# Performance work log

Measured on AMD Instinct MI355X. Metric: run time of the kernel, lower is better.

The kernel has to match this reference:

```python
import jax, jax.numpy as jnp
import numpy as np

B, S, D = 1, 2048, 2048
H, KVH, HD = 16, 8, 128
ROPE_THETA = 1e6
P_POW, C_SHIFT = 8, 7.0
MASK_VAL = -7.0  # = -c so masked bpmax base ~ scores only (finite under ^8)


def rotate_half(x):
    x1, x2 = jnp.split(x, 2, axis=-1)
    return jnp.concatenate([-x2, x1], axis=-1)


def setup_inputs() -> dict:
    key = jax.random.key(0)
    ks = jax.random.split(key, 10)
    hidden_states = jax.random.normal(ks[0], (B, S, D), dtype=jnp.float32)
    # RoPE tables (Qwen3-style, theta=1e6)
    inv_freq = 1.0 / (ROPE_THETA ** (jnp.arange(0, HD, 2, dtype=jnp.float32) / HD))
    freqs = jnp.arange(S, dtype=jnp.float32)[:, None] * inv_freq[None, :]
    emb = jnp.concatenate([freqs, freqs], axis=-1)  # [S, HD]
    cos = jnp.broadcast_to(jnp.cos(emb)[None], (B, S, HD)).astype(jnp.float32)
    sin = jnp.broadcast_to(jnp.sin(emb)[None], (B, S, HD)).astype(jnp.float32)
    sc = D ** -0.5
    q_proj_w = jax.random.normal(ks[1], (D, H * HD), dtype=jnp.float32) * sc
    k_proj_w = jax.random.normal(ks[2], (D, KVH * HD), dtype=jnp.float32) * sc
    v_proj_w = jax.random.normal(ks[3], (D, KVH * HD), dtype=jnp.float32) * sc
    o_proj_w = jax.random.normal(ks[4], (H * HD, D), dtype=jnp.float32) * (H * HD) ** -0.5
    q_norm_w = jnp.ones((HD,), dtype=jnp.float32)
    k_norm_w = jnp.ones((HD,), dtype=jnp.float32)
    # Stored RMSNorm denominators (rsqrt-like buffers from training), ~O(1)
    q_denom = 0.5 + jax.random.uniform(ks[5], (B, S, H, 1), dtype=jnp.float32)
    k_denom = 0.5 + jax.random.uniform(ks[6], (B, S, KVH, 1), dtype=jnp.float32)
    # Stored bpmax normalizer buffer rd (per-head, per-query-row)
    rd = 5.0 + 10.0 * jax.random.uniform(ks[7], (1, H, S, 1), dtype=jnp.float32)
    # Causal mask with MASK_VAL for masked positions (finite under bpmax)
    causal = jnp.tril(jnp.ones((S, S), dtype=bool))
    attention_mask = jnp.where(causal, 0.0, MASK_VAL)[None, None].astype(jnp.float32)
    return {
        'hidden_states': hidden_states, 'cos': cos, 'sin': sin,
        'q_proj_w': q_proj_w, 'k_proj_w': k_proj_w, 'v_proj_w': v_proj_w,
        'o_proj_w': o_proj_w, 'q_norm_w': q_norm_w, 'k_norm_w': k_norm_w,
        'q_denom': q_denom, 'k_denom': k_denom, 'rd': rd,
        'attention_mask': attention_mask,
    }


def reference(hidden_states, cos, sin, q_proj_w, k_proj_w, v_proj_w, o_proj_w,
              q_norm_w, k_norm_w, q_denom, k_denom, rd, attention_mask):
    b, s, d = hidden_states.shape
    hd = q_norm_w.shape[0]
    scaling = hd ** -0.5
    # Projections + per-head RMSNorm (eval path: stored denominator buffer)
    q = (hidden_states @ q_proj_w).reshape(b, s, -1, hd)
    q = (q_norm_w * (q * q_denom[:, :s])).transpose(0, 2, 1, 3)   # [B,H,S,hd]
    k = (hidden_states @ k_proj_w).reshape(b, s, -1, hd)
    k = (k_norm_w * (k * k_denom[:, :s])).transpose(0, 2, 1, 3)   # [B,KVH,S,hd]
    v = (hidden_states @ v_proj_w).reshape(b, s, -1, hd).transpose(0, 2, 1, 3)
    # RoPE
    cos_ = cos[:, None, :, :]
    sin_ = sin[:, None, :, :]
    q = q * cos_ + rotate_half(q) * sin_
    k = k * cos_ + rotate_half(k) * sin_
    # GQA: repeat kv heads
    groups = q.shape[1] // k.shape[1]
    k = jnp.repeat(k, groups, axis=1)
    v = jnp.repeat(v, groups, axis=1)
    # Scores + mask + bpmax power-law normalization (eval path)
    aw = jnp.einsum('bhqd,bhkd->bhqk', q, k) * scaling
    aw = aw + attention_mask[:, :, :, :s]
    aw = ((aw + C_SHIFT) / rd[:, :, :s, :]) ** P_POW
    # Attention output + output projection
    out = jnp.einsum('bhqk,bhkd->bhqd', aw, v)
    out = out.transpose(0, 2, 1, 3).reshape(b, s, -1)
    return out @ o_proj_w
```

## Files before the change

### kernel.cpp

```cpp
#include <hip/hip_runtime.h>
#include <cstdint>
#include <cstddef>


namespace {
constexpr int kS = 2048;
constexpr int kD = 2048;
constexpr int kH = 16;
constexpr int kKVH = 8;
constexpr int kHD = 128;
constexpr float kScale = 0.08838834764831845f;
constexpr size_t MB = 1u << 20;
}

using f32x4 = __attribute__((ext_vector_type(4))) float;
using bfrag = __attribute__((ext_vector_type(8))) short;
using float4v = __attribute__((ext_vector_type(4))) float;
using short4v = __attribute__((ext_vector_type(4))) short;

__device__ __forceinline__ unsigned short f2b(float f) {
  union { float f; unsigned u; } x; x.f = f;
  unsigned r = x.u + 0x7FFFu + ((x.u >> 16) & 1u);
  return (unsigned short)(r >> 16);
}

__device__ __forceinline__ void gload_lds16(const void* g, void* l) {
  __builtin_amdgcn_global_load_lds(
      (const __attribute__((address_space(1))) unsigned*)g,
      (__attribute__((address_space(3))) unsigned*)l, 16, 0, 0);
}

__global__ __launch_bounds__(256) void qwen_cast_bf16(const float* __restrict__ in,
                                                      unsigned short* __restrict__ out,
                                                      int n4) {
  int i = blockIdx.x * 256 + threadIdx.x;
  if (i >= n4) return;
  float4v v = *(const float4v*)(in + (size_t)i * 4);
  short4v o;
  o[0] = (short)f2b(v[0]); o[1] = (short)f2b(v[1]);
  o[2] = (short)f2b(v[2]); o[3] = (short)f2b(v[3]);
  int i4 = i * 4;
  int row = i4 >> 11, col = i4 & 2047;
  int scol = col ^ ((row & 3) << 3);
  *(short4v*)(out + ((size_t)row << 11) + scol) = o;
}

__global__ __launch_bounds__(256) void qwen_tw(const float* __restrict__ in, int R, int C,
                                               unsigned short* __restrict__ out, int ldo) {
  __shared__ float t[64][65];
  int c0 = blockIdx.x * 64, r0 = blockIdx.y * 64;
  int tr = threadIdx.x >> 6, tc = threadIdx.x & 63;
#pragma unroll
  for (int p = 0; p < 16; ++p) {
    int i = p * 4 + tr;
    t[i][tc] = in[(size_t)(r0 + i) * C + c0 + tc];
  }
  __syncthreads();
#pragma unroll
  for (int p = 0; p < 16; ++p) {
    int i = p * 4 + tr;
    int orow = c0 + i;
    int ocol = r0 + tc;
    int scol = ocol ^ ((orow & 3) << 3);
    out[(size_t)orow * ldo + scol] = f2b(t[tc][i]);
  }
}

template <int BM>
__global__ __launch_bounds__(256) void qwen_gemm_bt(const unsigned short* __restrict__ A,
                                                    const unsigned short* __restrict__ Bt,
                                                    float* __restrict__ C,
                                                    int M, int N, int K) {
  __shared__ unsigned short As[2][BM * 32];
  __shared__ unsigned short Bs[2][128 * 32];
  constexpr int MR = BM / 32;
  const int nwg = gridDim.x * gridDim.y;
  int lin = blockIdx.y * gridDim.x + blockIdx.x;
  if ((nwg & 7) == 0) { int qq = nwg >> 3; lin = (lin & 7) * qq + (lin >> 3); }
  const int bxx = lin % gridDim.x, byy = lin / gridDim.x;
  const int tid = threadIdx.x, lane = tid & 63, w = tid >> 6;
  const int wr = w >> 1, wc = w & 1;
  const int row0 = bxx * BM, col0 = byy * 128;
  f32x4 acc[MR][4] = {};
  const int koff = (lane >> 4) << 3;
  const int swz = (lane & 3) << 3;
  const int kread = koff ^ swz;
  const int rA = wr * (BM / 2) + (lane & 15);
  const int rB = wc * 64 + (lane & 15);

  auto stage = [&](int kt, int b) {
#pragma unroll
    for (int c = 0; c < BM / 64; ++c) {
      int off = (c * 256 + tid) * 16;
      int e = off >> 1;
      int r = e >> 5, cc = e & 31;
      gload_lds16(A + (size_t)(row0 + r) * K + kt + cc, (char*)(&As[b][0]) + off);
    }
#pragma unroll
    for (int c = 0; c < 2; ++c) {
      int off = (c * 256 + tid) * 16;
      int e = off >> 1;
      int r = e >> 5, cc = e & 31;
      gload_lds16(Bt + (size_t)(col0 + r) * K + kt + cc, (char*)(&Bs[b][0]) + off);
    }
  };

  const int nk = K >> 5;
  stage(0, 0);
  asm volatile("s_waitcnt vmcnt(0)" ::: "memory");
  __builtin_amdgcn_s_barrier();
  int buf = 0;
#pragma unroll 1
  for (int t = 0; t < nk; ++t) {
    if (t + 1 < nk) stage((t + 1) << 5, buf ^ 1);
    bfrag aF[MR], bF[4];
#pragma unroll
    for (int m = 0; m < MR; ++m)
      aF[m] = *(const bfrag*)(&As[buf][0] + (rA + m * 16) * 32 + kread);
#pragma unroll
    for (int n = 0; n < 4; ++n)
      bF[n] = *(const bfrag*)(&Bs[buf][0] + (rB + n * 16) * 32 + kread);
#pragma unroll
    for (int m = 0; m < MR; ++m)
#pragma unroll
      for (int n = 0; n < 4; ++n)
        acc[m][n] = __builtin_amdgcn_mfma_f32_16x16x32_bf16(aF[m], bF[n], acc[m][n], 0, 0, 0);
    asm volatile("s_waitcnt vmcnt(0)" ::: "memory");
    __builtin_amdgcn_s_barrier();
    buf ^= 1;
  }
  const int cr = (lane >> 4) << 2;
  const int cc2 = lane & 15;
#pragma unroll
  for (int m = 0; m < MR; ++m)
#pragma unroll
    for (int n = 0; n < 4; ++n) {
      int r = row0 + wr * (BM / 2) + m * 16 + cr;
      int c = col0 + wc * 64 + n * 16 + cc2;
#pragma unroll
      for (int j = 0; j < 4; ++j) C[(size_t)(r + j) * N + c] = acc[m][n][j];
    }
}

__global__ __launch_bounds__(256) void qwen_rope_qk(const float* __restrict__ Cqkv,
                                                    const float* __restrict__ cosb,
                                                    const float* __restrict__ sinb,
                                                    const float* __restrict__ qnw,
                                                    const float* __restrict__ knw,
                                                    const float* __restrict__ qden,
                                                    const float* __restrict__ kden,
                                                    unsigned short* __restrict__ Qb,
                                                    unsigned short* __restrict__ Kswz) {
  int s = blockIdx.x;
  int t = threadIdx.x;
  const float* row = Cqkv + (size_t)s * 4096;
  const float* cs = cosb + (size_t)s * kHD;
  const float* sn = sinb + (size_t)s * kHD;
#pragma unroll
  for (int rep = 0; rep < 8; ++rep) {
    int idx = rep * 256 + t;
    int h = idx >> 7, d = idx & 127;
    float dn = qden[s * kH + h];
    float v = row[idx] * dn * qnw[d];
    float pv = row[(h << 7) + (d ^ 64)] * dn * qnw[d ^ 64];
    float rot = (d < 64) ? -pv : pv;
    Qb[((size_t)h * kS + s) * kHD + d] = f2b(v * cs[d] + rot * sn[d]);
  }
  const int kt = s >> 6, key = s & 63;
#pragma unroll
  for (int rep = 0; rep < 4; ++rep) {
    int idx = rep * 256 + t;
    int h = idx >> 7, d = idx & 127;
    float dn = kden[s * kKVH + h];
    float v = row[2048 + idx] * dn * knw[d];
    float pv = row[2048 + (h << 7) + (d ^ 64)] * dn * knw[d ^ 64];
    float rot = (d < 64) ? -pv : pv;
    size_t rowi = ((size_t)(h * 32 + kt) * 64 + key) * 128;
    Kswz[rowi + (d ^ ((key & 7) << 3))] = f2b(v * cs[d] + rot * sn[d]);
  }
}

__global__ __launch_bounds__(256) void qwen_vtr(const float* __restrict__ Cqkv,
                                                unsigned short* __restrict__ Vswz) {
  __shared__ float t[64][65];
  int kvh = blockIdx.x, st = blockIdx.y, dt = blockIdx.z;
  int s0 = st * 64, d0 = dt * 64;
  int tr = threadIdx.x >> 6, tc = threadIdx.x & 63;
#pragma unroll
  for (int p = 0; p < 16; ++p) {
    int i = p * 4 + tr;
    t[i][tc] = Cqkv[(size_t)(s0 + i) * 4096 + 3072 + (kvh << 7) + d0 + tc];
  }
  __syncthreads();
#pragma unroll
  for (int p = 0; p < 16; ++p) {
    int i = p * 4 + tr;
    int d = d0 + i;
    size_t rowi = ((size_t)(kvh * 32 + st) * 128 + d) * 64;
    Vswz[rowi + (tc ^ ((d & 15) << 2))] = f2b(t[tc][i]);
  }
}

#define STAGE8(cc, bb)                                                 \
  do {                                                                 \
    const char* ks_ = Ksrc + ((size_t)(cc) << 14) + tid * 16;          \
    const char* vs_ = Vsrc + ((size_t)(cc) << 14) + tid * 16;          \
    char* kd_ = (char*)(&KV[bb][0]) + tid * 16;                        \
    char* vd_ = (char*)(&KV[2 + (bb)][0]) + tid * 16;                  \
    _Pragma("unroll") for (int it = 0; it < 4; ++it) {                 \
      gload_lds16(ks_ + it * 4096, kd_ + it * 4096);                   \
      gload_lds16(vs_ + it * 4096, vd_ + it * 4096);                   \
    }                                                                  \
  } while (0)

__global__ __launch_bounds__(256, 2) void qwen_attn(const unsigned short* __restrict__ Qb,
                                                    const unsigned short* __restrict__ Kswz,
                                                    const unsigned short* __restrict__ Vswz,
                                                    const float* __restrict__ rd,
                                                    unsigned short* __restrict__ AO) {
  __shared__ unsigned short KV[4][8192];
  const int bid = blockIdx.x;
  const int kvh = bid & 7;
  const int u = (bid >> 3) & 31;
  const int v = bid >> 8;
  const int h = kvh * 2 + (u & 1);
  const int j = u >> 1;
  const int qt = v ? j : (31 - j);
  const int q0 = qt * 64;
  const int nch = qt + 1;
  const int tid = threadIdx.x, lane = tid & 63, w = tid >> 6;
  const int l15 = lane & 15, g = lane >> 4;
  const int qw0 = q0 + w * 16;
  const int qlim = qw0 + l15;
  const int swzK = (l15 & 7) << 3;
  const int swzV = l15 << 2;

  bfrag qF[4];
#pragma unroll
  for (int dc = 0; dc < 4; ++dc)
    qF[dc] = *(const bfrag*)(Qb + ((size_t)h * kS + qw0 + l15) * kHD + dc * 32 + g * 8);
  const float inv = 1.0f / rd[(size_t)h * kS + qw0 + l15];

  const char* Ksrc = (const char*)Kswz + ((size_t)(kvh * 32) << 14);
  const char* Vsrc = (const char*)Vswz + ((size_t)(kvh * 32) << 14);

  f32x4 outa[8] = {};

  STAGE8(0, 0);
#pragma unroll 1
  for (int c = 0; c < nch; ++c) {
    const int b = c & 1;
    asm volatile("s_waitcnt vmcnt(0)" ::: "memory");
    __builtin_amdgcn_s_barrier();
    if (c + 1 < nch) STAGE8(c + 1, b ^ 1);
    __builtin_amdgcn_s_setprio(1);
    const unsigned short* Kbuf = &KV[b][0];
    const unsigned short* Vbuf = &KV[2 + b][0];
    f32x4 sc[4] = {};
#pragma unroll
    for (int t = 0; t < 4; ++t) {
      const unsigned short* kr = Kbuf + (t * 16 + l15) * 128;
#pragma unroll
      for (int dc = 0; dc < 4; ++dc) {
        bfrag kf = *(const bfrag*)(kr + ((dc * 32 + g * 8) ^ swzK));
        sc[t] = __builtin_amdgcn_mfma_f32_16x16x32_bf16(kf, qF[dc], sc[t], 0, 0, 0);
      }
    }
    const int kbase = c * 64;
    const bool full = (c < qt);
    union { bfrag f; unsigned u[4]; } pb[2];
#pragma unroll
    for (int t = 0; t < 4; ++t) {
      unsigned short bb[4];
#pragma unroll
      for (int rr = 0; rr < 4; ++rr) {
        float tt = sc[t][rr] * kScale;
        int key = kbase + t * 16 + g * 4 + rr;
        tt += (full || key <= qlim) ? 7.0f : 0.0f;
        float y = tt * inv;
        float y2 = y * y, y4 = y2 * y2;
        bb[rr] = f2b(y4 * y4);
      }
      pb[t >> 1].u[(t & 1) * 2 + 0] = (unsigned)bb[0] | ((unsigned)bb[1] << 16);
      pb[t >> 1].u[(t & 1) * 2 + 1] = (unsigned)bb[2] | ((unsigned)bb[3] << 16);
    }
#pragma unroll
    for (int dt = 0; dt < 8; ++dt) {
      const unsigned short* vr = Vbuf + (dt * 16 + l15) * 64;
#pragma unroll
      for (int pr = 0; pr < 2; ++pr) {
        union { bfrag f; short4v h4[2]; } va;
        va.h4[0] = *(const short4v*)(vr + ((pr * 32 + g * 4) ^ swzV));
        va.h4[1] = *(const short4v*)(vr + ((pr * 32 + 16 + g * 4) ^ swzV));
        outa[dt] = __builtin_amdgcn_mfma_f32_16x16x32_bf16(va.f, pb[pr].f, outa[dt], 0, 0, 0);
      }
    }
    __builtin_amdgcn_s_setprio(0);
  }
  {
    const int swzA = (l15 & 3) << 3;
#pragma unroll
    for (int dt = 0; dt < 8; ++dt) {
      short4v o;
      o[0] = (short)f2b(outa[dt][0]); o[1] = (short)f2b(outa[dt][1]);
      o[2] = (short)f2b(outa[dt][2]); o[3] = (short)f2b(outa[dt][3]);
      int col = h * 128 + dt * 16 + g * 4;
      *(short4v*)(AO + (size_t)(qw0 + l15) * kD + (col ^ swzA)) = o;
    }
  }
}

extern "C" void kernel_launch(void* const* d_in, const int* in_sizes, int n_in,
                              void* d_out, int out_size, void* d_ws, size_t ws_size,
                              hipStream_t stream) {
  (void)in_sizes; (void)n_in; (void)out_size; (void)ws_size;
  const float* hidden = (const float*)d_in[0];
  const float* cosb   = (const float*)d_in[1];
  const float* sinb   = (const float*)d_in[2];
  const float* qw     = (const float*)d_in[3];
  const float* kw     = (const float*)d_in[4];
  const float* vw     = (const float*)d_in[5];
  const float* ow     = (const float*)d_in[6];
  const float* qnw    = (const float*)d_in[7];
  const float* knw    = (const float*)d_in[8];
  const float* qden   = (const float*)d_in[9];
  const float* kden   = (const float*)d_in[10];
  const float* rd     = (const float*)d_in[11];
  float* out = (float*)d_out;

  char* ws = (char*)d_ws;
  unsigned short* hsb  = (unsigned short*)(ws + 0 * MB);
  unsigned short* Wt   = (unsigned short*)(ws + 8 * MB);
  float*          Cqkv = (float*)(ws + 24 * MB);
  unsigned short* Qb   = (unsigned short*)(ws + 56 * MB);
  unsigned short* Kswz = (unsigned short*)(ws + 64 * MB);
  unsigned short* Vswz = (unsigned short*)(ws + 68 * MB);
  unsigned short* AO   = (unsigned short*)(ws + 72 * MB);
  unsigned short* Ot   = (unsigned short*)(ws + 80 * MB);

  qwen_cast_bf16<<<4096, 256, 0, stream>>>(hidden, hsb, 2048 * 2048 / 4);
  qwen_tw<<<dim3(32, 32), 256, 0, stream>>>(qw, 2048, 2048, Wt, 2048);
  qwen_tw<<<dim3(16, 32), 256, 0, stream>>>(kw, 2048, 1024, Wt + (size_t)2048 * 2048, 2048);
  qwen_tw<<<dim3(16, 32), 256, 0, stream>>>(vw, 2048, 1024, Wt + (size_t)3072 * 2048, 2048);
  qwen_tw<<<dim3(32, 32), 256, 0, stream>>>(ow, 2048, 2048, Ot, 2048);
  qwen_gemm_bt<128><<<dim3(16, 32), 256, 0, stream>>>(hsb, Wt, Cqkv, 2048, 4096, 2048);
  qwen_rope_qk<<<2048, 256, 0, stream>>>(Cqkv, cosb, sinb, qnw, knw, qden, kden, Qb, Kswz);
  qwen_vtr<<<dim3(8, 32, 2), 256, 0, stream>>>(Cqkv, Vswz);
  qwen_attn<<<512, 256, 0, stream>>>(Qb, Kswz, Vswz, rd, AO);
  qwen_gemm_bt<128><<<dim3(16, 16), 256, 0, stream>>>(AO, Ot, out, 2048, 2048, 2048);
}
```

Baseline: 169.5 us.

## Fuse RoPE, norm scaling and V transpose into QKV GEMM epilogue

Replaces the generic QKV GEMM, the separate RoPE/norm kernel and the V transpose kernel with one GEMM whose epilogue applies the denominator, norm weight and RoPE, writing bf16 Q/K/V straight into the swizzled layouts. The rotate-half partner value is exchanged through shared memory, which reuses the staging buffer after the main loop. This removes the 32 MB fp32 intermediate round trip and two kernel launches. In exchange the epilogue does scattered 2-byte stores and adds shared-memory pressure (64 KB), which may lower occupancy.

```diff
diff --git a/kernel.cpp b/kernel.cpp
--- a/kernel.cpp
+++ b/kernel.cpp
@@ -142,62 +142,136 @@
     }
 }
 
-__global__ __launch_bounds__(256) void qwen_rope_qk(const float* __restrict__ Cqkv,
-                                                    const float* __restrict__ cosb,
-                                                    const float* __restrict__ sinb,
-                                                    const float* __restrict__ qnw,
-                                                    const float* __restrict__ knw,
-                                                    const float* __restrict__ qden,
-                                                    const float* __restrict__ kden,
-                                                    unsigned short* __restrict__ Qb,
-                                                    unsigned short* __restrict__ Kswz) {
-  int s = blockIdx.x;
-  int t = threadIdx.x;
-  const float* row = Cqkv + (size_t)s * 4096;
-  const float* cs = cosb + (size_t)s * kHD;
-  const float* sn = sinb + (size_t)s * kHD;
-#pragma unroll
-  for (int rep = 0; rep < 8; ++rep) {
-    int idx = rep * 256 + t;
-    int h = idx >> 7, d = idx & 127;
-    float dn = qden[s * kH + h];
-    float v = row[idx] * dn * qnw[d];
-    float pv = row[(h << 7) + (d ^ 64)] * dn * qnw[d ^ 64];
-    float rot = (d < 64) ? -pv : pv;
-    Qb[((size_t)h * kS + s) * kHD + d] = f2b(v * cs[d] + rot * sn[d]);
-  }
-  const int kt = s >> 6, key = s & 63;
-#pragma unroll
-  for (int rep = 0; rep < 4; ++rep) {
-    int idx = rep * 256 + t;
-    int h = idx >> 7, d = idx & 127;
-    float dn = kden[s * kKVH + h];
-    float v = row[2048 + idx] * dn * knw[d];
-    float pv = row[2048 + (h << 7) + (d ^ 64)] * dn * knw[d ^ 64];
-    float rot = (d < 64) ? -pv : pv;
-    size_t rowi = ((size_t)(h * 32 + kt) * 64 + key) * 128;
-    Kswz[rowi + (d ^ ((key & 7) << 3))] = f2b(v * cs[d] + rot * sn[d]);
-  }
-}
-
-__global__ __launch_bounds__(256) void qwen_vtr(const float* __restrict__ Cqkv,
-                                                unsigned short* __restrict__ Vswz) {
-  __shared__ float t[64][65];
-  int kvh = blockIdx.x, st = blockIdx.y, dt = blockIdx.z;
-  int s0 = st * 64, d0 = dt * 64;
-  int tr = threadIdx.x >> 6, tc = threadIdx.x & 63;
-#pragma unroll
-  for (int p = 0; p < 16; ++p) {
-    int i = p * 4 + tr;
-    t[i][tc] = Cqkv[(size_t)(s0 + i) * 4096 + 3072 + (kvh << 7) + d0 + tc];
-  }
-  __syncthreads();
-#pragma unroll
-  for (int p = 0; p < 16; ++p) {
-    int i = p * 4 + tr;
-    int d = d0 + i;
-    size_t rowi = ((size_t)(kvh * 32 + st) * 128 + d) * 64;
-    Vswz[rowi + (tc ^ ((d & 15) << 2))] = f2b(t[tc][i]);
+__global__ __launch_bounds__(256) void qwen_gemm_qkv(const unsigned short* __restrict__ A,
+                                                     const unsigned short* __restrict__ Bt,
+                                                     const float* __restrict__ cosb,
+                                                     const float* __restrict__ sinb,
+                                                     const float* __restrict__ qnw,
+                                                     const float* __restrict__ knw,
+                                                     const float* __restrict__ qden,
+                                                     const float* __restrict__ kden,
+                                                     unsigned short* __restrict__ Qb,
+                                                     unsigned short* __restrict__ Kswz,
+                                                     unsigned short* __restrict__ Vswz) {
+  __shared__ char smem[65536];
+  unsigned short(*As)[128 * 32] = (unsigned short(*)[128 * 32])smem;
+  unsigned short(*Bs)[128 * 32] = (unsigned short(*)[128 * 32])(smem + 16384);
+  float(*ex)[256] = (float(*)[256])smem;
+  constexpr int K = 2048, N = 4096;
+  const int nwg = gridDim.x * gridDim.y;
+  int lin = blockIdx.y * gridDim.x + blockIdx.x;
+  { int qq = nwg >> 3; lin = (lin & 7) * qq + (lin >> 3); }
+  const int bxx = lin % gridDim.x, byy = lin / gridDim.x;
+  const int tid = threadIdx.x, lane = tid & 63, w = tid >> 6;
+  const int wr = w >> 1, wc = w & 1;
+  const int row0 = bxx * 128;
+  const int col0 = byy * 128;
+  f32x4 acc[4][4] = {};
+  const int koff = (lane >> 4) << 3;
+  const int kread = koff ^ ((lane & 3) << 3);
+  const int rA = wr * 64 + (lane & 15);
+  const int rB = wc * 64 + (lane & 15);
+
+  auto stage = [&](int kt, int b) {
+#pragma unroll
+    for (int c = 0; c < 2; ++c) {
+      int off = (c * 256 + tid) * 16;
+      int e = off >> 1;
+      int r = e >> 5, cc = e & 31;
+      gload_lds16(A + (size_t)(row0 + r) * K + kt + cc, (char*)(&As[b][0]) + off);
+    }
+#pragma unroll
+    for (int c = 0; c < 2; ++c) {
+      int off = (c * 256 + tid) * 16;
+      int e = off >> 1;
+      int r = e >> 5, cc = e & 31;
+      gload_lds16(Bt + (size_t)(col0 + r) * K + kt + cc, (char*)(&Bs[b][0]) + off);
+    }
+  };
+
+  const int nk = K >> 5;
+  stage(0, 0);
+  asm volatile("s_waitcnt vmcnt(0)" ::: "memory");
+  __builtin_amdgcn_s_barrier();
+  int buf = 0;
+#pragma unroll 1
+  for (int t = 0; t < nk; ++t) {
+    if (t + 1 < nk) stage((t + 1) << 5, buf ^ 1);
+    bfrag aF[4], bF[4];
+#pragma unroll
+    for (int m = 0; m < 4; ++m)
+      aF[m] = *(const bfrag*)(&As[buf][0] + (rA + m * 16) * 32 + kread);
+#pragma unroll
+    for (int n = 0; n < 4; ++n)
+      bF[n] = *(const bfrag*)(&Bs[buf][0] + (rB + n * 16) * 32 + kread);
+#pragma unroll
+    for (int m = 0; m < 4; ++m)
+#pragma unroll
+      for (int n = 0; n < 4; ++n)
+        acc[m][n] = __builtin_amdgcn_mfma_f32_16x16x32_bf16(aF[m], bF[n], acc[m][n], 0, 0, 0);
+    asm volatile("s_waitcnt vmcnt(0)" ::: "memory");
+    __builtin_amdgcn_s_barrier();
+    buf ^= 1;
+  }
+
+  const int cr = (lane >> 4) << 2;
+  const int cc2 = lane & 15;
+  if (byy >= 24) {
+    const int kvh = byy - 24;
+#pragma unroll
+    for (int m = 0; m < 4; ++m)
+#pragma unroll
+      for (int n = 0; n < 4; ++n) {
+        int s = row0 + wr * 64 + m * 16 + cr;
+        int d = wc * 64 + n * 16 + cc2;
+        int st = s >> 6, key = s & 63;
+        size_t rowi = ((size_t)(kvh * 32 + st) * 128 + d) * 64;
+        short4v o;
+        o[0] = (short)f2b(acc[m][n][0]); o[1] = (short)f2b(acc[m][n][1]);
+        o[2] = (short)f2b(acc[m][n][2]); o[3] = (short)f2b(acc[m][n][3]);
+        *(short4v*)(Vswz + rowi + (key ^ ((d & 15) << 2))) = o;
+      }
+  } else {
+#pragma unroll
+    for (int m = 0; m < 4; ++m)
+#pragma unroll
+      for (int n = 0; n < 4; ++n)
+#pragma unroll
+        for (int j = 0; j < 4; ++j)
+          ex[(m * 4 + n) * 4 + j][tid] = acc[m][n][j];
+    __syncthreads();
+    const bool isQ = (byy < 16);
+    const int hh = isQ ? byy : (byy - 16);
+    const float* nw = isQ ? qnw : knw;
+    const float* den = isQ ? qden : kden;
+    const int H = isQ ? 16 : 8;
+#pragma unroll
+    for (int m = 0; m < 4; ++m) {
+#pragma unroll
+      for (int n = 0; n < 4; ++n) {
+        const int d = wc * 64 + n * 16 + cc2;
+        const float nwd = nw[d], nwp = nw[d ^ 64];
+        const int d63 = d & 63;
+#pragma unroll
+        for (int j = 0; j < 4; ++j) {
+          int s = row0 + wr * 64 + m * 16 + cr + j;
+          float dn = den[s * H + hh];
+          float cs = cosb[s * kHD + d63];
+          float sn = sinb[s * kHD + d63];
+          float v = acc[m][n][j] * dn * nwd;
+          float pv = ex[(m * 4 + n) * 4 + j][tid ^ 64] * dn * nwp;
+          float rot = (d < 64) ? -pv : pv;
+          unsigned short ob = f2b(v * cs + rot * sn);
+          if (isQ) {
+            Qb[((size_t)hh * kS + s) * kHD + d] = ob;
+          } else {
+            int kt = s >> 6, key = s & 63;
+            size_t rowi = ((size_t)(hh * 32 + kt) * 64 + key) * 128;
+            Kswz[rowi + (d ^ ((key & 7) << 3))] = ob;
+          }
+        }
+      }
+    }
   }
 }
 
@@ -331,7 +405,6 @@
   char* ws = (char*)d_ws;
   unsigned short* hsb  = (unsigned short*)(ws + 0 * MB);
   unsigned short* Wt   = (unsigned short*)(ws + 8 * MB);
-  float*          Cqkv = (float*)(ws + 24 * MB);
   unsigned short* Qb   = (unsigned short*)(ws + 56 * MB);
   unsigned short* Kswz = (unsigned short*)(ws + 64 * MB);
   unsigned short* Vswz = (unsigned short*)(ws + 68 * MB);
@@ -343,9 +416,8 @@
   qwen_tw<<<dim3(16, 32), 256, 0, stream>>>(kw, 2048, 1024, Wt + (size_t)2048 * 2048, 2048);
   qwen_tw<<<dim3(16, 32), 256, 0, stream>>>(vw, 2048, 1024, Wt + (size_t)3072 * 2048, 2048);
   qwen_tw<<<dim3(32, 32), 256, 0, stream>>>(ow, 2048, 2048, Ot, 2048);
-  qwen_gemm_bt<128><<<dim3(16, 32), 256, 0, stream>>>(hsb, Wt, Cqkv, 2048, 4096, 2048);
-  qwen_rope_qk<<<2048, 256, 0, stream>>>(Cqkv, cosb, sinb, qnw, knw, qden, kden, Qb, Kswz);
-  qwen_vtr<<<dim3(8, 32, 2), 256, 0, stream>>>(Cqkv, Vswz);
+  qwen_gemm_qkv<<<dim3(16, 32), 256, 0, stream>>>(hsb, Wt, cosb, sinb, qnw, knw,
+                                                  qden, kden, Qb, Kswz, Vswz);
   qwen_attn<<<512, 256, 0, stream>>>(Qb, Kswz, Vswz, rd, AO);
   qwen_gemm_bt<128><<<dim3(16, 16), 256, 0, stream>>>(AO, Ot, out, 2048, 2048, 2048);
 }
```

Result: faster. 165.1 us (-2.6%).
